# Kernel optimization log

Hardware: AMD Instinct MI355X
Metric: run time of the kernel (lower is better)

Reference implementation:

```python
import jax, jax.numpy as jnp
import numpy as np
from jax import lax

GAMMA = 0.1  # fixed RBF bandwidth from LearnableRBFInfluence


def setup_inputs() -> dict:
    key = jax.random.key(0)
    k1, k2, k3, k4 = jax.random.split(key, 4)
    B, H, W = 2, 256, 256
    NUM_FILTERS, KS, NUM_BASIS = 48, 7, 31
    u_log = jax.random.normal(k1, (B, 1, H, W), jnp.float32)
    f_log = jax.random.normal(k2, (B, 1, H, W), jnp.float32)
    filters = jax.random.normal(k3, (NUM_FILTERS, 1, KS, KS), jnp.float32) * 0.05
    rbf_weights = jax.random.normal(k4, (NUM_FILTERS, NUM_BASIS), jnp.float32) * 0.05
    lambda_param = jnp.float32(0.1)
    return {"u_log": u_log, "f_log": f_log, "filters": filters,
            "rbf_weights": rbf_weights, "lambda_param": lambda_param}


def reference(u_log, f_log, filters, rbf_weights, lambda_param):
    # Batched form of the per-filter loop:
    #   conv[i] = conv2d(u, k_i)  ->  one grouped conv with 48 output channels
    num_basis = rbf_weights.shape[1]
    mu = jnp.linspace(-1.0, 1.0, num_basis).astype(u_log.dtype)  # [K]

    dn = lax.conv_dimension_numbers(u_log.shape, filters.shape, ('NCHW', 'OIHW', 'NCHW'))
    conv = lax.conv_general_dilated(u_log, filters, (1, 1), 'SAME',
                                    dimension_numbers=dn)  # [B,48,H,W]

    # RBF influence, per filter channel c: phi = sum_k w[c,k] * exp(-(conv-mu_k)^2/(2 g^2))
    diff = conv[..., None] - mu                              # [B,48,H,W,K]
    rbf = jnp.exp(-(diff * diff) / (2.0 * GAMMA * GAMMA))
    phi = jnp.einsum('bchwk,ck->bchw', rbf, rbf_weights)     # [B,48,H,W]

    # Per-filter conv2d(phi_i, flip(k_i)) summed over i == single conv
    # with OIHW weight [1,48,7,7] built from spatially-flipped filters.
    kT = jnp.flip(filters, axis=(2, 3)).transpose(1, 0, 2, 3)  # [1,48,7,7]
    dn2 = lax.conv_dimension_numbers(phi.shape, kT.shape, ('NCHW', 'OIHW', 'NCHW'))
    diffusion = lax.conv_general_dilated(phi, kT, (1, 1), 'SAME',
                                         dimension_numbers=dn2)  # [B,1,H,W]

    reaction = lambda_param * (u_log - f_log)
    return u_log - diffusion - reaction
```

## Files before the change

### kernel.cpp

```cpp
#include <hip/hip_runtime.h>

#define HH 256
#define WW 256
#define NPIX (2 * HH * WW)
#define NC 48
#define NB 31
#define NG 6
#define CG 8
#define OT 32
#define PT 38
#define PSTR 44
#define UT 44
#define USTR 52
#define TM 385
#define TSTR 386

__global__ __launch_bounds__(256)
void tnrd_table(const float* __restrict__ wr, float* __restrict__ tab)
{
    const int ch = blockIdx.x;
    const float* rc = wr + ch * NB;
    for (int j = threadIdx.x; j < TSTR; j += 256) {
        float x = fmaf((float)j, 3.0f / 384.0f, -1.5f);
        float s = 0.f;
        #pragma unroll
        for (int k = 0; k < NB; ++k) {
            float mu = -1.f + (float)k * (1.f / 15.f);
            float d = x - mu;
            s = fmaf(rc[k], __expf(-50.f * d * d), s);
        }
        tab[ch * TSTR + j] = s;
    }
}

__global__ __launch_bounds__(256, 3)
void tnrd_main(const float* __restrict__ u,
               const float* __restrict__ wf,
               const float* __restrict__ tab,
               float* __restrict__ part)
{
    __shared__ __align__(16) float u_s[UT * USTR];
    __shared__ __align__(16) float phi_s[4][PT * PSTR];
    __shared__ __align__(16) float tabs[CG][TSTR];

    const int tid = threadIdx.x;
    const int bx = blockIdx.x, by = blockIdx.y;
    const int b = blockIdx.z / NG, g = blockIdx.z % NG;
    const int c0g = g * CG;

    const int uy0 = by * OT - 6, ux0 = bx * OT - 6;
    const float* ub = u + b * (HH * WW);
    for (int i = tid; i < UT * USTR; i += 256) {
        int r = i / USTR, c = i - r * USTR;
        int gy = uy0 + r, gx = ux0 + c;
        float v = 0.f;
        if (c < UT && (unsigned)gy < HH && (unsigned)gx < WW)
            v = ub[gy * WW + gx];
        u_s[i] = v;
    }

    {
        const float4* src = (const float4*)(tab + c0g * TSTR);
        float4* dst = (float4*)&tabs[0][0];
        #pragma unroll 1
        for (int i = tid; i < CG * TSTR / 4; i += 256) dst[i] = src[i];
    }

    const int oy = tid >> 3;
    const int ox0 = (tid & 7) * 4;
    float o0 = 0.f, o1 = 0.f, o2 = 0.f, o3 = 0.f;
    const int py0 = by * OT - 3, px0 = bx * OT - 3;

    auto conv1_pass = [&](int cp, float* __restrict__ bufA,
                          float* __restrict__ bufB) {
        const float* wA = wf + (c0g + 2 * cp) * 49;
        const float* wB = wA + 49;
        const float* tA = tabs[2 * cp];
        const float* tB = tabs[2 * cp + 1];
        for (int p = 0; p < 2; ++p) {
            const int gi = tid + p * 256;
            if (gi < PT * 10) {
                const int pr = gi % PT, pc = (gi / PT) * 4;
                float a0 = 0.f, a1 = 0.f, a2 = 0.f, a3 = 0.f;
                float b0 = 0.f, b1 = 0.f, b2 = 0.f, b3 = 0.f;
                const float* bptr = &u_s[pr * USTR + pc];

                auto fmab = [&](const float* wa, const float* wb,
                                float4 q0, float4 q1, float4 q2) {
                    float sv[12] = {q0.x, q0.y, q0.z, q0.w,
                                    q1.x, q1.y, q1.z, q1.w,
                                    q2.x, q2.y, q2.z, q2.w};
                    #pragma unroll
                    for (int dx = 0; dx < 7; ++dx) {
                        float fa = wa[dx], fb = wb[dx];
                        a0 = fmaf(sv[dx],     fa, a0);
                        a1 = fmaf(sv[dx + 1], fa, a1);
                        a2 = fmaf(sv[dx + 2], fa, a2);
                        a3 = fmaf(sv[dx + 3], fa, a3);
                        b0 = fmaf(sv[dx],     fb, b0);
                        b1 = fmaf(sv[dx + 1], fb, b1);
                        b2 = fmaf(sv[dx + 2], fb, b2);
                        b3 = fmaf(sv[dx + 3], fb, b3);
                    }
                };

                float4 c0 = *(const float4*)(bptr);
                float4 c1 = *(const float4*)(bptr + 4);
                float4 c2 = *(const float4*)(bptr + 8);
                #pragma unroll 1
                for (int dy = 0; dy < 6; ++dy) {
                    const float* nr = bptr + (dy + 1) * USTR;
                    float4 n0 = *(const float4*)(nr);
                    float4 n1 = *(const float4*)(nr + 4);
                    float4 n2 = *(const float4*)(nr + 8);
                    fmab(wA + dy * 7, wB + dy * 7, c0, c1, c2);
                    c0 = n0; c1 = n1; c2 = n2;
                }
                fmab(wA + 42, wB + 42, c0, c1, c2);

                const int gy = py0 + pr;
                const bool rowok = (unsigned)gy < HH;
                float av[4] = {a0, a1, a2, a3};
                float bv[4] = {b0, b1, b2, b3};
                float pha[4], phb[4];
                #pragma unroll
                for (int j = 0; j < 4; ++j) {
                    bool ok = rowok && (unsigned)(px0 + pc + j) < WW;
                    float ta = fminf(fmaxf(fmaf(av[j], 128.f, 192.f), 0.f), 383.999f);
                    float fja = floorf(ta);
                    int ia = (int)fja;
                    float va = fmaf(ta - fja, tA[ia + 1] - tA[ia], tA[ia]);
                    float tb = fminf(fmaxf(fmaf(bv[j], 128.f, 192.f), 0.f), 383.999f);
                    float fjb = floorf(tb);
                    int ib = (int)fjb;
                    float vb = fmaf(tb - fjb, tB[ib + 1] - tB[ib], tB[ib]);
                    pha[j] = ok ? va : 0.f;
                    phb[j] = ok ? vb : 0.f;
                }
                float* dA = bufA + pr * PSTR + pc;
                float* dB = bufB + pr * PSTR + pc;
                #pragma unroll
                for (int j = 0; j < 4; ++j) dA[j] = pha[j];
                #pragma unroll
                for (int j = 0; j < 4; ++j) dB[j] = phb[j];
            }
        }
    };

    conv1_pass(0, phi_s[0], phi_s[1]);
    __syncthreads();

    #pragma unroll 1
    for (int pass = 0; pass < 4; ++pass) {
        if (pass < 3) {
            const int nb_ = (pass + 1) & 1;
            conv1_pass(pass + 1, phi_s[2 * nb_], phi_s[2 * nb_ + 1]);
        }

        const float* wA = wf + (c0g + 2 * pass) * 49;
        const float* wB = wA + 49;
        const float* pA = phi_s[2 * (pass & 1)];
        const float* pB = phi_s[2 * (pass & 1) + 1];
        for (int dy = 0; dy < 7; ++dy) {
            const float* rA = pA + (oy + dy) * PSTR + ox0;
            const float* rB = pB + (oy + dy) * PSTR + ox0;
            float sa[10], sb[10];
            #pragma unroll
            for (int j = 0; j < 10; ++j) sa[j] = rA[j];
            #pragma unroll
            for (int j = 0; j < 10; ++j) sb[j] = rB[j];
            #pragma unroll
            for (int dx = 0; dx < 7; ++dx) {
                float fa = wA[(6 - dy) * 7 + (6 - dx)];
                float fb = wB[(6 - dy) * 7 + (6 - dx)];
                o0 = fmaf(sa[dx],     fa, o0);
                o1 = fmaf(sa[dx + 1], fa, o1);
                o2 = fmaf(sa[dx + 2], fa, o2);
                o3 = fmaf(sa[dx + 3], fa, o3);
                o0 = fmaf(sb[dx],     fb, o0);
                o1 = fmaf(sb[dx + 1], fb, o1);
                o2 = fmaf(sb[dx + 2], fb, o2);
                o3 = fmaf(sb[dx + 3], fb, o3);
            }
        }
        if (pass < 3) __syncthreads();
    }

    const int gy = by * OT + oy, gx = bx * OT + ox0;
    float4 v4 = make_float4(o0, o1, o2, o3);
    *reinterpret_cast<float4*>(part + (size_t)g * NPIX + b * (HH * WW)
                               + gy * WW + gx) = v4;
}

__global__ __launch_bounds__(256)
void combine_kernel(const float* __restrict__ u,
                    const float* __restrict__ f,
                    const float* __restrict__ lam,
                    const float* __restrict__ part,
                    float* __restrict__ out)
{
    int i = blockIdx.x * 256 + threadIdx.x;
    float d = 0.f;
    #pragma unroll
    for (int g = 0; g < NG; ++g) d += part[g * NPIX + i];
    float lv = lam[0];
    float uv = u[i];
    float fv = f[i];
    out[i] = uv - d - lv * (uv - fv);
}

extern "C" void kernel_launch(void* const* d_in, const int* in_sizes, int n_in,
                              void* d_out, int out_size, void* d_ws, size_t ws_size,
                              hipStream_t stream) {
    const float* u    = (const float*)d_in[0];
    const float* f    = (const float*)d_in[1];
    const float* filt = (const float*)d_in[2];
    const float* rbfw = (const float*)d_in[3];
    const float* lam  = (const float*)d_in[4];
    float* out = (float*)d_out;
    float* part = (float*)d_ws;
    float* tabg = (float*)d_out;

    tnrd_table<<<NC, 256, 0, stream>>>(rbfw, tabg);
    tnrd_main<<<dim3(8, 8, 2 * NG), 256, 0, stream>>>(u, filt, tabg, part);
    combine_kernel<<<512, 256, 0, stream>>>(u, f, lam, part, out);
}
```

Before: 109.9 us.

## Fuse group reduction and combine into main kernel via atomics and last-block epilogue

Replaces the per-group partial buffer and separate combine kernel with float atomicAdds into a single accumulator. A per-tile counter is incremented, and the last of the six group blocks for each tile computes the final u - d - lambda*(u-f) output. This removes one kernel launch and the write and re-read of six partial images. In exchange it adds a memset, atomic traffic and fences, and makes the floating-point summation order nondeterministic.

Result: slower. 144.3 us (+31.3%).

```diff
diff --git a/kernel.cpp b/kernel.cpp
--- a/kernel.cpp
+++ b/kernel.cpp
@@ -14,6 +14,9 @@
 #define USTR 52
 #define TM 385
 #define TSTR 386
+#define NTILE 128
+#define CNT_OFF  NPIX
+#define TAB_OFF  (NPIX + NTILE)
 
 __global__ __launch_bounds__(256)
 void tnrd_table(const float* __restrict__ wr, float* __restrict__ tab)
@@ -35,13 +38,18 @@
 
 __global__ __launch_bounds__(256, 3)
 void tnrd_main(const float* __restrict__ u,
+               const float* __restrict__ fimg,
+               const float* __restrict__ lam,
                const float* __restrict__ wf,
                const float* __restrict__ tab,
-               float* __restrict__ part)
+               float* __restrict__ acc,
+               unsigned* __restrict__ cnt,
+               float* __restrict__ outp)
 {
     __shared__ __align__(16) float u_s[UT * USTR];
     __shared__ __align__(16) float phi_s[4][PT * PSTR];
     __shared__ __align__(16) float tabs[CG][TSTR];
+    __shared__ int last_flag;
 
     const int tid = threadIdx.x;
     const int bx = blockIdx.x, by = blockIdx.y;
@@ -187,26 +195,34 @@
     }
 
     const int gy = by * OT + oy, gx = bx * OT + ox0;
-    float4 v4 = make_float4(o0, o1, o2, o3);
-    *reinterpret_cast<float4*>(part + (size_t)g * NPIX + b * (HH * WW)
-                               + gy * WW + gx) = v4;
-}
-
-__global__ __launch_bounds__(256)
-void combine_kernel(const float* __restrict__ u,
-                    const float* __restrict__ f,
-                    const float* __restrict__ lam,
-                    const float* __restrict__ part,
-                    float* __restrict__ out)
-{
-    int i = blockIdx.x * 256 + threadIdx.x;
-    float d = 0.f;
-    #pragma unroll
-    for (int g = 0; g < NG; ++g) d += part[g * NPIX + i];
-    float lv = lam[0];
-    float uv = u[i];
-    float fv = f[i];
-    out[i] = uv - d - lv * (uv - fv);
+    const int base = b * (HH * WW) + gy * WW + gx;
+    atomicAdd(&acc[base + 0], o0);
+    atomicAdd(&acc[base + 1], o1);
+    atomicAdd(&acc[base + 2], o2);
+    atomicAdd(&acc[base + 3], o3);
+    __threadfence();
+    __syncthreads();
+    if (tid == 0) {
+        unsigned old = atomicAdd(&cnt[b * 64 + by * 8 + bx], 1u);
+        last_flag = (old == NG - 1) ? 1 : 0;
+    }
+    __syncthreads();
+    if (last_flag) {
+        __threadfence();
+        float lv = lam[0];
+        float4 uv4 = *(const float4*)(u + base);
+        float4 fv4 = *(const float4*)(fimg + base);
+        float d0 = atomicAdd(&acc[base + 0], 0.f);
+        float d1 = atomicAdd(&acc[base + 1], 0.f);
+        float d2 = atomicAdd(&acc[base + 2], 0.f);
+        float d3 = atomicAdd(&acc[base + 3], 0.f);
+        float4 r;
+        r.x = uv4.x - d0 - lv * (uv4.x - fv4.x);
+        r.y = uv4.y - d1 - lv * (uv4.y - fv4.y);
+        r.z = uv4.z - d2 - lv * (uv4.z - fv4.z);
+        r.w = uv4.w - d3 - lv * (uv4.w - fv4.w);
+        *(float4*)(outp + base) = r;
+    }
 }
 
 extern "C" void kernel_launch(void* const* d_in, const int* in_sizes, int n_in,
@@ -218,10 +234,13 @@
     const float* rbfw = (const float*)d_in[3];
     const float* lam  = (const float*)d_in[4];
     float* out = (float*)d_out;
-    float* part = (float*)d_ws;
-    float* tabg = (float*)d_out;
-
+    float* ws  = (float*)d_ws;
+    float*    acc  = ws;
+    unsigned* cnt  = (unsigned*)(ws + CNT_OFF);
+    float*    tabg = ws + TAB_OFF;
+
+    hipMemsetAsync(d_ws, 0, (size_t)(NPIX + NTILE) * sizeof(float), stream);
     tnrd_table<<<NC, 256, 0, stream>>>(rbfw, tabg);
-    tnrd_main<<<dim3(8, 8, 2 * NG), 256, 0, stream>>>(u, filt, tabg, part);
-    combine_kernel<<<512, 256, 0, stream>>>(u, f, lam, part, out);
+    tnrd_main<<<dim3(8, 8, 2 * NG), 256, 0, stream>>>(u, f, lam, filt, tabg,
+                                                      acc, cnt, out);
 }
```
